# Performance work log

Hardware: AMD Instinct MI355X
Metric: run time of the kernel (lower is better)

## Reference

```python
import jax, jax.numpy as jnp
import numpy as np

F8 = jnp.float8_e4m3fn  # e4m3 max normal = 448.0, matching the torch clamp


def setup_inputs() -> dict:
    key = jax.random.key(0)
    k1, k2, k3 = jax.random.split(key, 3)
    B, T, C, O = 2, 4096, 4096, 16384
    x = jax.random.normal(k1, (B, T, C), dtype=jnp.float32)
    W = jax.random.normal(k2, (O, C), dtype=jnp.float32) * 0.02  # nn.Linear-style weight [out, in]
    bias = jax.random.normal(k3, (O,), dtype=jnp.float32) * 0.02
    return {"x": x, "W": W, "bias": bias}


def reference(x, W, bias):
    # QuantLinear.forward with quant_type='fp8', biasmode=True:
    #   Qweight = weight.to(float8_e4m3fn); out = scaled_mm(clamp(x,-448,448).to(fp8), Qweight.t()) + bias
    # Emulated as fp8 quantize->dequantize on both operands, then a fp32 GEMM
    # (scale_a = scale_b = 1.0 in the original, out_dtype = x.dtype).
    xq = jnp.clip(x, -448.0, 448.0).astype(F8).astype(jnp.float32)   # [B,T,C]
    Wq = W.astype(F8).astype(jnp.float32)                             # [O,C]
    out = jnp.einsum('btc,oc->bto', xq, Wq) + bias                    # [B,T,O]
    return out
```

## Files before the change

### kernel.cpp

```cpp
#include <hip/hip_runtime.h>
#include <stdint.h>

#define TILE 128
#define BK 32

typedef float f32x4 __attribute__((ext_vector_type(4)));
typedef const __attribute__((address_space(1))) void* gp1_t;
typedef __attribute__((address_space(3))) void* lp3_t;

__device__ __forceinline__ void gload_lds16(const void* g, void* l) {
  __builtin_amdgcn_global_load_lds((gp1_t)g, (lp3_t)l, 16, 0, 0);
}

__device__ __forceinline__ uint32_t pack4_fp8(float a, float b, float c, float d) {
  a = fminf(fmaxf(a, -448.f), 448.f);
  b = fminf(fmaxf(b, -448.f), 448.f);
  c = fminf(fmaxf(c, -448.f), 448.f);
  d = fminf(fmaxf(d, -448.f), 448.f);
  uint32_t v = 0;
  v = __builtin_amdgcn_cvt_pk_fp8_f32(a, b, v, false);
  v = __builtin_amdgcn_cvt_pk_fp8_f32(c, d, v, true);
  return v;
}

__global__ __launch_bounds__(256) void quant_fp8(const float* __restrict__ in,
                                                 uint4* __restrict__ out) {
  size_t t = (size_t)blockIdx.x * 256 + threadIdx.x;
  const float4* in4 = (const float4*)in;
  float4 v0 = in4[t * 4 + 0];
  float4 v1 = in4[t * 4 + 1];
  float4 v2 = in4[t * 4 + 2];
  float4 v3 = in4[t * 4 + 3];
  uint4 r;
  r.x = pack4_fp8(v0.x, v0.y, v0.z, v0.w);
  r.y = pack4_fp8(v1.x, v1.y, v1.z, v1.w);
  r.z = pack4_fp8(v2.x, v2.y, v2.z, v2.w);
  r.w = pack4_fp8(v3.x, v3.y, v3.z, v3.w);
  out[t] = r;
}

__global__ __launch_bounds__(256) void gemm_fp8(const uint8_t* __restrict__ A,
                                                const uint8_t* __restrict__ B,
                                                const float* __restrict__ bias,
                                                float* __restrict__ C,
                                                int M, int N, int K) {
  __shared__ uint8_t As[TILE * BK];
  __shared__ uint8_t Bs[TILE * BK];

  const int num_n = N / TILE;
  const int GM = 16;
  int bid = blockIdx.x;
  int per_group = GM * num_n;
  int group = bid / per_group;
  int rem = bid - group * per_group;
  int tile_m = group * GM + (rem % GM);
  int tile_n = rem / GM;

  const int tid = threadIdx.x;
  const int wave = tid >> 6;
  const int lane = tid & 63;

  const size_t m0 = (size_t)tile_m * TILE;
  const size_t n0 = (size_t)tile_n * TILE;

  const int srow = tid >> 1;
  const int scol = (tid & 1) * 16;
  const uint8_t* agp = A + (m0 + srow) * (size_t)K + scol;
  const uint8_t* bgp = B + (n0 + srow) * (size_t)K + scol;
  uint8_t* alds = As + wave * 1024;
  uint8_t* blds = Bs + wave * 1024;

  const int wm = wave & 1;
  const int wn = wave >> 1;
  const int lm = lane & 15;
  const int quad = lane >> 4;

  f32x4 acc[4][4] = {};

  int a_off[4], b_off[4];
#pragma unroll
  for (int i = 0; i < 4; ++i) {
    a_off[i] = (wm * 64 + i * 16 + lm) * BK + quad * 8;
    b_off[i] = (wn * 64 + i * 16 + lm) * BK + quad * 8;
  }

  for (int kt = 0; kt < K; kt += BK) {
    gload_lds16(agp + kt, alds);
    gload_lds16(bgp + kt, blds);
    __syncthreads();
    long af[4], bf[4];
#pragma unroll
    for (int i = 0; i < 4; ++i) af[i] = *(const long*)(As + a_off[i]);
#pragma unroll
    for (int j = 0; j < 4; ++j) bf[j] = *(const long*)(Bs + b_off[j]);
#pragma unroll
    for (int i = 0; i < 4; ++i)
#pragma unroll
      for (int j = 0; j < 4; ++j)
        acc[i][j] = __builtin_amdgcn_mfma_f32_16x16x32_fp8_fp8(af[i], bf[j], acc[i][j], 0, 0, 0);
    __syncthreads();
  }

  const int row_base = (int)m0 + wm * 64 + quad * 4;
  const int col_base = (int)n0 + wn * 64 + lm;
#pragma unroll
  for (int j = 0; j < 4; ++j) {
    int col = col_base + j * 16;
    float bv = bias[col];
#pragma unroll
    for (int i = 0; i < 4; ++i) {
      int row = row_base + i * 16;
#pragma unroll
      for (int r = 0; r < 4; ++r) {
        __builtin_nontemporal_store(acc[i][j][r] + bv, C + (size_t)(row + r) * N + col);
      }
    }
  }
}

extern "C" void kernel_launch(void* const* d_in, const int* in_sizes, int n_in,
                              void* d_out, int out_size, void* d_ws, size_t ws_size,
                              hipStream_t stream) {
  const float* x = (const float*)d_in[0];
  const float* W = (const float*)d_in[1];
  const float* bias = (const float*)d_in[2];
  float* out = (float*)d_out;

  const int N = in_sizes[2];
  const int K = in_sizes[1] / N;
  const int M = in_sizes[0] / K;

  uint8_t* Xq = (uint8_t*)d_ws;
  uint8_t* Wq = Xq + (size_t)M * K;

  {
    int blocks_x = (int)(((size_t)M * K) / (16 * 256));
    quant_fp8<<<blocks_x, 256, 0, stream>>>(x, (uint4*)Xq);
    int blocks_w = (int)(((size_t)N * K) / (16 * 256));
    quant_fp8<<<blocks_w, 256, 0, stream>>>(W, (uint4*)Wq);
  }

  int grid = (M / TILE) * (N / TILE);
  gemm_fp8<<<grid, 256, 0, stream>>>(Xq, Wq, bias, out, M, N, K);
}
```

Measured before the change: 1.912 ms.

## Rewrite FP8 GEMM with 256x256 tiles, 4-stage LDS pipeline and swizzle

Replaces the single-buffered 128x128 GEMM with a 512-thread 256x256 tile kernel that prefetches three K-tiles ahead into a 4-slot LDS ring via direct global-to-LDS loads. The LDS layout is XOR-swizzled to avoid bank conflicts, and the MFMA work is split into four quadrant phases interleaved with staged loads and s_setprio. Workgroups are remapped across XCDs for better L2 locality. This is meant to hide memory latency and raise compute intensity, at the cost of 128KB of LDS, heavy register use and intricate waitcnt/barrier logic.

New measurement: 1.969 ms. 1.03x slower.

```diff
diff --git a/kernel.cpp b/kernel.cpp
--- a/kernel.cpp
+++ b/kernel.cpp
@@ -1,8 +1,5 @@
 #include <hip/hip_runtime.h>
 #include <stdint.h>
-
-#define TILE 128
-#define BK 32
 
 typedef float f32x4 __attribute__((ext_vector_type(4)));
 typedef const __attribute__((address_space(1))) void* gp1_t;
@@ -39,80 +36,185 @@
   out[t] = r;
 }
 
-__global__ __launch_bounds__(256) void gemm_fp8(const uint8_t* __restrict__ A,
-                                                const uint8_t* __restrict__ B,
-                                                const float* __restrict__ bias,
-                                                float* __restrict__ C,
-                                                int M, int N, int K) {
-  __shared__ uint8_t As[TILE * BK];
-  __shared__ uint8_t Bs[TILE * BK];
-
-  const int num_n = N / TILE;
-  const int GM = 16;
-  int bid = blockIdx.x;
-  int per_group = GM * num_n;
-  int group = bid / per_group;
-  int rem = bid - group * per_group;
-  int tile_m = group * GM + (rem % GM);
-  int tile_n = rem / GM;
+#define BM 256
+#define BN 256
+#define BKT 64
+#define BUFSZ 32768
+#define BOFF 16384
+
+__global__ __launch_bounds__(512, 2) void gemm_fp8(const uint8_t* __restrict__ A,
+                                                   const uint8_t* __restrict__ B,
+                                                   const float* __restrict__ bias,
+                                                   float* __restrict__ C,
+                                                   int M, int N, int K) {
+  __shared__ uint8_t lds[4 * BUFSZ];
+
+  const int num_m = M / BM;
+  const int num_n = N / BN;
+
+  const int nwg = num_m * num_n;
+  const int cpx = nwg >> 3;
+  const int bid = blockIdx.x;
+  const int swz = (bid & 7) * cpx + (bid >> 3);
+  const int tile_m = swz % num_m;
+  const int tile_n = swz / num_m;
 
   const int tid = threadIdx.x;
-  const int wave = tid >> 6;
   const int lane = tid & 63;
-
-  const size_t m0 = (size_t)tile_m * TILE;
-  const size_t n0 = (size_t)tile_n * TILE;
-
-  const int srow = tid >> 1;
-  const int scol = (tid & 1) * 16;
-  const uint8_t* agp = A + (m0 + srow) * (size_t)K + scol;
-  const uint8_t* bgp = B + (n0 + srow) * (size_t)K + scol;
-  uint8_t* alds = As + wave * 1024;
-  uint8_t* blds = Bs + wave * 1024;
-
-  const int wm = wave & 1;
-  const int wn = wave >> 1;
+  const int wid = tid >> 6;
+  const int wm = wid >> 2;
+  const int wn = wid & 3;
   const int lm = lane & 15;
   const int quad = lane >> 4;
 
-  f32x4 acc[4][4] = {};
-
-  int a_off[4], b_off[4];
-#pragma unroll
-  for (int i = 0; i < 4; ++i) {
-    a_off[i] = (wm * 64 + i * 16 + lm) * BK + quad * 8;
-    b_off[i] = (wn * 64 + i * 16 + lm) * BK + quad * 8;
-  }
-
-  for (int kt = 0; kt < K; kt += BK) {
-    gload_lds16(agp + kt, alds);
-    gload_lds16(bgp + kt, blds);
-    __syncthreads();
-    long af[4], bf[4];
-#pragma unroll
-    for (int i = 0; i < 4; ++i) af[i] = *(const long*)(As + a_off[i]);
-#pragma unroll
-    for (int j = 0; j < 4; ++j) bf[j] = *(const long*)(Bs + b_off[j]);
-#pragma unroll
-    for (int i = 0; i < 4; ++i)
-#pragma unroll
-      for (int j = 0; j < 4; ++j)
-        acc[i][j] = __builtin_amdgcn_mfma_f32_16x16x32_fp8_fp8(af[i], bf[j], acc[i][j], 0, 0, 0);
-    __syncthreads();
-  }
-
-  const int row_base = (int)m0 + wm * 64 + quad * 4;
+  const size_t m0 = (size_t)tile_m * BM;
+  const size_t n0 = (size_t)tile_n * BN;
+
+  const int srow = tid >> 2;
+  const int spc = (tid & 3) << 4;
+  const int scol = spc ^ ((srow & 3) << 4);
+  const uint8_t* agA = A + (m0 + srow) * (size_t)K + scol;
+  const uint8_t* agB = B + (n0 + srow) * (size_t)K + scol;
+  const size_t halfK = (size_t)128 * K;
+
+  const int cs0 = (quad * 8) ^ ((lm & 3) << 4);
+  const int cs1 = (32 + quad * 8) ^ ((lm & 3) << 4);
+  const int arow = (wm * 128 + lm) * 64;
+  const int brow = BOFF + (wn * 64 + lm) * 64;
+
+  f32x4 acc[8][4] = {};
+  long a[8], bl[4], bh[4];
+
+  const int NT = K >> 6;
+
+  for (int t = 0; t < 3; ++t) {
+    uint8_t* buf = lds + t * BUFSZ;
+    const uint8_t* ka = agA + (size_t)t * BKT;
+    const uint8_t* kb = agB + (size_t)t * BKT;
+    gload_lds16(ka, buf + tid * 16);
+    gload_lds16(ka + halfK, buf + 8192 + tid * 16);
+    gload_lds16(kb, buf + BOFF + tid * 16);
+    gload_lds16(kb + halfK, buf + BOFF + 8192 + tid * 16);
+  }
+  asm volatile("s_waitcnt vmcnt(8)" ::: "memory");
+  __builtin_amdgcn_s_barrier();
+
+  for (int t = 0; t < NT; ++t) {
+    const uint8_t* bufc = lds + (t & 3) * BUFSZ;
+    uint8_t* bufs = lds + ((t + 3) & 3) * BUFSZ;
+    const bool do_stage = (t + 3) < NT;
+    const uint8_t* ka = agA + (size_t)(t + 3) * BKT;
+    const uint8_t* kb = agB + (size_t)(t + 3) * BKT;
+    const uint8_t* pa0 = bufc + arow + cs0;
+    const uint8_t* pa1 = bufc + arow + cs1;
+    const uint8_t* pb0 = bufc + brow + cs0;
+    const uint8_t* pb1 = bufc + brow + cs1;
+
+#pragma unroll
+    for (int i = 0; i < 4; ++i) {
+      a[i * 2 + 0] = *(const long*)(pa0 + i * 1024);
+      a[i * 2 + 1] = *(const long*)(pa1 + i * 1024);
+    }
+#pragma unroll
+    for (int j = 0; j < 2; ++j) {
+      bl[j * 2 + 0] = *(const long*)(pb0 + j * 1024);
+      bl[j * 2 + 1] = *(const long*)(pb1 + j * 1024);
+    }
+    if (do_stage) gload_lds16(ka, bufs + tid * 16);
+    asm volatile("" ::: "memory");
+    __builtin_amdgcn_s_barrier();
+    asm volatile("s_waitcnt lgkmcnt(0)" ::: "memory");
+    __builtin_amdgcn_s_setprio(1);
+#pragma unroll
+    for (int ks = 0; ks < 2; ++ks)
+#pragma unroll
+      for (int i = 0; i < 4; ++i)
+#pragma unroll
+        for (int j = 0; j < 2; ++j)
+          acc[i][j] = __builtin_amdgcn_mfma_f32_16x16x32_fp8_fp8(
+              a[i * 2 + ks], bl[j * 2 + ks], acc[i][j], 0, 0, 0);
+    __builtin_amdgcn_s_setprio(0);
+    __builtin_amdgcn_s_barrier();
+
+#pragma unroll
+    for (int j = 0; j < 2; ++j) {
+      bh[j * 2 + 0] = *(const long*)(pb0 + 2048 + j * 1024);
+      bh[j * 2 + 1] = *(const long*)(pb1 + 2048 + j * 1024);
+    }
+    if (do_stage) gload_lds16(ka + halfK, bufs + 8192 + tid * 16);
+    asm volatile("" ::: "memory");
+    __builtin_amdgcn_s_barrier();
+    asm volatile("s_waitcnt lgkmcnt(0)" ::: "memory");
+    __builtin_amdgcn_s_setprio(1);
+#pragma unroll
+    for (int ks = 0; ks < 2; ++ks)
+#pragma unroll
+      for (int i = 0; i < 4; ++i)
+#pragma unroll
+        for (int j = 0; j < 2; ++j)
+          acc[i][2 + j] = __builtin_amdgcn_mfma_f32_16x16x32_fp8_fp8(
+              a[i * 2 + ks], bh[j * 2 + ks], acc[i][2 + j], 0, 0, 0);
+    __builtin_amdgcn_s_setprio(0);
+    __builtin_amdgcn_s_barrier();
+
+#pragma unroll
+    for (int i = 0; i < 4; ++i) {
+      a[i * 2 + 0] = *(const long*)(pa0 + 4096 + i * 1024);
+      a[i * 2 + 1] = *(const long*)(pa1 + 4096 + i * 1024);
+    }
+    if (do_stage) gload_lds16(kb, bufs + BOFF + tid * 16);
+    asm volatile("" ::: "memory");
+    __builtin_amdgcn_s_barrier();
+    asm volatile("s_waitcnt lgkmcnt(0)" ::: "memory");
+    __builtin_amdgcn_s_setprio(1);
+#pragma unroll
+    for (int ks = 0; ks < 2; ++ks)
+#pragma unroll
+      for (int i = 0; i < 4; ++i)
+#pragma unroll
+        for (int j = 0; j < 2; ++j)
+          acc[4 + i][2 + j] = __builtin_amdgcn_mfma_f32_16x16x32_fp8_fp8(
+              a[i * 2 + ks], bh[j * 2 + ks], acc[4 + i][2 + j], 0, 0, 0);
+    __builtin_amdgcn_s_setprio(0);
+    __builtin_amdgcn_s_barrier();
+
+    if (do_stage) gload_lds16(kb + halfK, bufs + BOFF + 8192 + tid * 16);
+    asm volatile("" ::: "memory");
+    __builtin_amdgcn_s_barrier();
+    asm volatile("s_waitcnt lgkmcnt(0)" ::: "memory");
+    __builtin_amdgcn_s_setprio(1);
+#pragma unroll
+    for (int ks = 0; ks < 2; ++ks)
+#pragma unroll
+      for (int i = 0; i < 4; ++i)
+#pragma unroll
+        for (int j = 0; j < 2; ++j)
+          acc[4 + i][j] = __builtin_amdgcn_mfma_f32_16x16x32_fp8_fp8(
+              a[i * 2 + ks], bl[j * 2 + ks], acc[4 + i][j], 0, 0, 0);
+    __builtin_amdgcn_s_setprio(0);
+    if (t < NT - 3) {
+      asm volatile("s_waitcnt vmcnt(8)" ::: "memory");
+    } else if (t == NT - 3) {
+      asm volatile("s_waitcnt vmcnt(4)" ::: "memory");
+    } else if (t == NT - 2) {
+      asm volatile("s_waitcnt vmcnt(0)" ::: "memory");
+    }
+    __builtin_amdgcn_s_barrier();
+  }
+
+  const int row_base = (int)m0 + wm * 128 + quad * 4;
   const int col_base = (int)n0 + wn * 64 + lm;
 #pragma unroll
-  for (int j = 0; j < 4; ++j) {
-    int col = col_base + j * 16;
+  for (int nj = 0; nj < 4; ++nj) {
+    int col = col_base + nj * 16;
     float bv = bias[col];
 #pragma unroll
-    for (int i = 0; i < 4; ++i) {
-      int row = row_base + i * 16;
+    for (int mi = 0; mi < 8; ++mi) {
+      int row = row_base + mi * 16;
 #pragma unroll
       for (int r = 0; r < 4; ++r) {
-        __builtin_nontemporal_store(acc[i][j][r] + bv, C + (size_t)(row + r) * N + col);
+        __builtin_nontemporal_store(acc[mi][nj][r] + bv,
+                                    C + (size_t)(row + r) * N + col);
       }
     }
   }
@@ -140,6 +242,6 @@
     quant_fp8<<<blocks_w, 256, 0, stream>>>(W, (uint4*)Wq);
   }
 
-  int grid = (M / TILE) * (N / TILE);
-  gemm_fp8<<<grid, 256, 0, stream>>>(Xq, Wq, bias, out, M, N, K);
-}
+  int grid = (M / BM) * (N / BN);
+  gemm_fp8<<<grid, 512, 0, stream>>>(Xq, Wq, bias, out, M, N, K);
+}
```
